# Kernel optimization log

Measured on AMD Instinct MI355X. Metric: run time of the kernel, lower is better.

The kernel has to match this reference:

```python
import jax, jax.numpy as jnp
import numpy as np

B, S, D_MODEL, D_K, D_V, H = 4, 2048, 1024, 1024, 1024, 16


def setup_inputs() -> dict:
    key = jax.random.key(0)
    ks = jax.random.split(key, 8)
    std_qk = np.sqrt(2.0 / (D_MODEL + D_K)).astype(np.float32)
    std_v = np.sqrt(2.0 / (D_MODEL + D_V)).astype(np.float32)
    std_o = np.sqrt(2.0 / (D_V + D_MODEL)).astype(np.float32)  # xavier normal
    return {
        "Q": jax.random.normal(ks[0], (B, S, D_MODEL), jnp.float32),
        "K": jax.random.normal(ks[1], (B, S, D_MODEL), jnp.float32),
        "V": jax.random.normal(ks[2], (B, S, D_MODEL), jnp.float32),
        "Wq": jax.random.normal(ks[3], (D_MODEL, D_K), jnp.float32) * std_qk,
        "bq": jnp.zeros((D_K,), jnp.float32),
        "Wk": jax.random.normal(ks[4], (D_MODEL, D_K), jnp.float32) * std_qk,
        "bk": jnp.zeros((D_K,), jnp.float32),
        "Wv": jax.random.normal(ks[5], (D_MODEL, D_V), jnp.float32) * std_v,
        "bv": jnp.zeros((D_V,), jnp.float32),
        "Wo": jax.random.normal(ks[6], (D_V, D_MODEL), jnp.float32) * std_o,
        "bo": jnp.zeros((D_MODEL,), jnp.float32),
    }


def reference(Q, K, V, Wq, bq, Wk, bk, Wv, bv, Wo, bo):
    b, s, _ = Q.shape
    hd = D_K // H  # per-head dim
    # separate QKV projections
    q = (Q @ Wq + bq).reshape(b, s, H, hd)
    k = (K @ Wk + bk).reshape(b, s, H, hd)
    v = (V @ Wv + bv).reshape(b, s, H, D_V // H)
    # scaled dot-product attention per head
    scale = 1.0 / jnp.sqrt(jnp.asarray(hd, Q.dtype))
    scores = jnp.einsum("bqhd,bkhd->bhqk", q, k) * scale
    attn = jax.nn.softmax(scores, axis=-1)
    o = jnp.einsum("bhqk,bkhd->bqhd", attn, v).reshape(b, s, D_V)
    # output projection
    return o @ Wo + bo
```

## Files before the change

kernel.cpp:

```cpp
#include <hip/hip_runtime.h>
#include <hip/hip_bf16.h>
#include <stdint.h>


#define B_  4
#define S_  2048
#define DM  1024
#define H_  16
#define HD  64
#define BH  (B_ * H_)

typedef __attribute__((ext_vector_type(8))) short short8;
typedef __attribute__((ext_vector_type(4))) float f32x4;

union U8 { short8 v; ushort u[8]; };

__device__ __forceinline__ ushort f2bf(float f) {
  union { float f; uint32_t i; } x; x.f = f;
  uint32_t r = (x.i + 0x7FFFu + ((x.i >> 16) & 1u)) >> 16;
  return (ushort)r;
}

__device__ __forceinline__ uint32_t cvt_pk_bf16(float a, float b) {
  uint32_t r;
  asm("v_cvt_pk_bf16_f32 %0, %1, %2" : "=v"(r) : "v"(a), "v"(b));
  return r;
}

__device__ __forceinline__ float exp2f_fast(float x) {
  float r;
  asm("v_exp_f32 %0, %1" : "=v"(r) : "v"(x));
  return r;
}

__device__ __forceinline__ void glds16(const ushort* g, ushort* l) {
  __builtin_amdgcn_global_load_lds(
      (const __attribute__((address_space(1))) void*)g,
      (__attribute__((address_space(3))) void*)l, 16, 0, 0);
}

#define MAX3(a, b, c) fmaxf(fmaxf((a), (b)), (c))

__global__ __launch_bounds__(256) void transposeW4(
    const float* __restrict__ s0, const float* __restrict__ s1,
    const float* __restrict__ s2, const float* __restrict__ s3,
    ushort* __restrict__ dbase) {
  __shared__ __align__(16) ushort tile[64][72];
  const int t = threadIdx.x;
  const int bx = blockIdx.x & 15;
  const int by = blockIdx.x >> 4;
  const int wsel = blockIdx.y;
  const float* src = wsel == 0 ? s0 : (wsel == 1 ? s1 : (wsel == 2 ? s2 : s3));
  ushort* dst = dbase + (size_t)wsel * 1024 * 1024;
#pragma unroll
  for (int i = 0; i < 2; i++) {
    int e = (i * 256 + t) * 8;
    int r = e >> 6, c = e & 63;
    const float* sp = src + (size_t)(by * 64 + r) * 1024 + bx * 64 + c;
    float4 a = ((const float4*)sp)[0];
    float4 b = ((const float4*)sp)[1];
    tile[r][c + 0] = f2bf(a.x); tile[r][c + 1] = f2bf(a.y);
    tile[r][c + 2] = f2bf(a.z); tile[r][c + 3] = f2bf(a.w);
    tile[r][c + 4] = f2bf(b.x); tile[r][c + 5] = f2bf(b.y);
    tile[r][c + 6] = f2bf(b.z); tile[r][c + 7] = f2bf(b.w);
  }
  __syncthreads();
#pragma unroll
  for (int i = 0; i < 2; i++) {
    int e = (i * 256 + t) * 8;
    int r = e >> 6, c = e & 63;
    U8 st;
#pragma unroll
    for (int j = 0; j < 8; j++) st.u[j] = tile[c + j][r];
    *(short8*)(dst + (size_t)(bx * 64 + r) * 1024 + by * 64 + c) = st.v;
  }
}


__global__ __launch_bounds__(256, 2) void gemm_qkv(
    const float* __restrict__ Qa, const float* __restrict__ Ka, const float* __restrict__ Va,
    const ushort* __restrict__ WT,
    const float* __restrict__ bq, const float* __restrict__ bk, const float* __restrict__ bv,
    ushort* __restrict__ qws, ushort* __restrict__ kws, ushort* __restrict__ vt) {
  __shared__ __align__(16) ushort lA[128 * 32];
  __shared__ __align__(16) ushort lB[128 * 32];
  const int z = blockIdx.z;
  const float* Ap = z == 0 ? Qa : (z == 1 ? Ka : Va);
  const ushort* BT = WT + (size_t)z * 1024 * 1024;
  const float* bias = z == 0 ? bq : (z == 1 ? bk : bv);
  const float oscale = z == 0 ? 0.18033688f : 1.0f;
  const int t = threadIdx.x;
  const int lane = t & 63;
  const int w = t >> 6;
  const int wr = w >> 1, wc = w & 1;
  const int bm0 = blockIdx.x * 128;
  const int bn0 = blockIdx.y * 128;
  f32x4 acc[4][4] = {};

  const int arow = t >> 2;
  const int acol = (t & 3) * 8;
  const int swz  = ((t & 3) ^ ((t >> 3) & 3)) * 8;
  const int rdo  = (((lane >> 4) ^ ((lane >> 1) & 3))) * 8;
  const float* fA0 = Ap + (size_t)(bm0 + arow) * 1024 + acol;
  const float* fA1 = Ap + (size_t)(bm0 + 64 + arow) * 1024 + acol;
  const ushort* gB0 = BT + (size_t)(bn0 + arow) * 1024 + swz;
  const ushort* gB1 = BT + (size_t)(bn0 + 64 + arow) * 1024 + swz;
  ushort* lAs0 = &lA[(t >> 2) * 32 + swz];
  ushort* lAs1 = &lA[2048 + (t >> 2) * 32 + swz];

  float4 px0 = ((const float4*)fA0)[0];
  float4 px1 = ((const float4*)fA0)[1];
  float4 py0 = ((const float4*)fA1)[0];
  float4 py1 = ((const float4*)fA1)[1];

  for (int k0 = 0; k0 < 1024; k0 += 32) {
    if (k0) __syncthreads();
    union { short8 v; uint32_t u[4]; } s0, s1;
    s0.u[0] = cvt_pk_bf16(px0.x, px0.y); s0.u[1] = cvt_pk_bf16(px0.z, px0.w);
    s0.u[2] = cvt_pk_bf16(px1.x, px1.y); s0.u[3] = cvt_pk_bf16(px1.z, px1.w);
    s1.u[0] = cvt_pk_bf16(py0.x, py0.y); s1.u[1] = cvt_pk_bf16(py0.z, py0.w);
    s1.u[2] = cvt_pk_bf16(py1.x, py1.y); s1.u[3] = cvt_pk_bf16(py1.z, py1.w);
    *(short8*)lAs0 = s0.v;
    *(short8*)lAs1 = s1.v;
    glds16(gB0 + k0, &lB[t * 8]);
    glds16(gB1 + k0, &lB[2048 + t * 8]);
    __syncthreads();
    if (k0 + 32 < 1024) {
      px0 = ((const float4*)(fA0 + k0 + 32))[0];
      px1 = ((const float4*)(fA0 + k0 + 32))[1];
      py0 = ((const float4*)(fA1 + k0 + 32))[0];
      py1 = ((const float4*)(fA1 + k0 + 32))[1];
    }
    short8 af[4], bf[4];
#pragma unroll
    for (int i = 0; i < 4; i++)
      af[i] = *(const short8*)&lA[(wr * 64 + i * 16 + (lane & 15)) * 32 + rdo];
#pragma unroll
    for (int j = 0; j < 4; j++)
      bf[j] = *(const short8*)&lB[(wc * 64 + j * 16 + (lane & 15)) * 32 + rdo];
#pragma unroll
    for (int i = 0; i < 4; i++)
#pragma unroll
      for (int j = 0; j < 4; j++)
        acc[i][j] = __builtin_amdgcn_mfma_f32_16x16x32_bf16(af[i], bf[j], acc[i][j], 0, 0, 0);
  }

  const int r0 = (lane >> 4) * 4;
#pragma unroll
  for (int j = 0; j < 4; j++) {
    const int col = bn0 + wc * 64 + j * 16 + (lane & 15);
    const float bc = bias[col];
#pragma unroll
    for (int i = 0; i < 4; i++) {
      const int row = bm0 + wr * 64 + i * 16 + r0;
      const int bb = row >> 11, s = row & 2047;
      const int hh = col >> 6, d = col & 63;
      if (z == 2) {
        uint32_t p01 = cvt_pk_bf16(acc[i][j][0] + bc, acc[i][j][1] + bc);
        uint32_t p23 = cvt_pk_bf16(acc[i][j][2] + bc, acc[i][j][3] + bc);
        ushort* vtb = vt + (((size_t)bb * H_ + hh) * HD + d) * (size_t)S_;
        const int sc = (s & 63) >> 2;
        *(uint2*)(vtb + (s & ~63) + ((sc ^ (d & 15)) << 2)) = (uint2){p01, p23};
      } else {
        ushort* dst = z == 0 ? qws : kws;
#pragma unroll
        for (int r = 0; r < 4; r++) {
          float val = (acc[i][j][r] + bc) * oscale;
          dst[(((size_t)bb * H_ + hh) * S_ + (s + r)) * HD + d] = f2bf(val);
        }
      }
    }
  }
}

__global__ __launch_bounds__(256, 2) void gemm_out(
    const ushort* __restrict__ Ap, const ushort* __restrict__ BT,
    const float* __restrict__ bias, float* __restrict__ Cp) {
  __shared__ __align__(16) ushort lA[128 * 32];
  __shared__ __align__(16) ushort lB[128 * 32];
  const int t = threadIdx.x;
  const int lane = t & 63;
  const int w = t >> 6;
  const int wr = w >> 1, wc = w & 1;
  const int bm0 = blockIdx.x * 128;
  const int bn0 = blockIdx.y * 128;
  f32x4 acc[4][4] = {};

  const int arow = t >> 2;
  const int swz  = ((t & 3) ^ ((t >> 3) & 3)) * 8;
  const int rdo  = (((lane >> 4) ^ ((lane >> 1) & 3))) * 8;
  const ushort* gA0 = Ap + (size_t)(bm0 + arow) * 1024 + swz;
  const ushort* gA1 = Ap + (size_t)(bm0 + 64 + arow) * 1024 + swz;
  const ushort* gB0 = BT + (size_t)(bn0 + arow) * 1024 + swz;
  const ushort* gB1 = BT + (size_t)(bn0 + 64 + arow) * 1024 + swz;

  for (int k0 = 0; k0 < 1024; k0 += 32) {
    if (k0) __syncthreads();
    glds16(gA0 + k0, &lA[t * 8]);
    glds16(gA1 + k0, &lA[2048 + t * 8]);
    glds16(gB0 + k0, &lB[t * 8]);
    glds16(gB1 + k0, &lB[2048 + t * 8]);
    __syncthreads();
    short8 af[4], bf[4];
#pragma unroll
    for (int i = 0; i < 4; i++)
      af[i] = *(const short8*)&lA[(wr * 64 + i * 16 + (lane & 15)) * 32 + rdo];
#pragma unroll
    for (int j = 0; j < 4; j++)
      bf[j] = *(const short8*)&lB[(wc * 64 + j * 16 + (lane & 15)) * 32 + rdo];
#pragma unroll
    for (int i = 0; i < 4; i++)
#pragma unroll
      for (int j = 0; j < 4; j++)
        acc[i][j] = __builtin_amdgcn_mfma_f32_16x16x32_bf16(af[i], bf[j], acc[i][j], 0, 0, 0);
  }

  const int r0 = (lane >> 4) * 4;
#pragma unroll
  for (int j = 0; j < 4; j++) {
    const int col = bn0 + wc * 64 + j * 16 + (lane & 15);
    const float bc = bias[col];
#pragma unroll
    for (int i = 0; i < 4; i++) {
      const int row = bm0 + wr * 64 + i * 16 + r0;
#pragma unroll
      for (int r = 0; r < 4; r++)
        Cp[(size_t)(row + r) * 1024 + col] = acc[i][j][r] + bc;
    }
  }
}

__global__ __launch_bounds__(256, 2) void attn(
    const ushort* __restrict__ q, const ushort* __restrict__ k,
    const ushort* __restrict__ vt, ushort* __restrict__ o) {
  __shared__ __align__(16) ushort kbuf[2][8192];
  __shared__ __align__(16) ushort vbuf[2][8192];
  const int t = threadIdx.x;
  const int lane = t & 63;
  const int w = t >> 6;
  const int L = ((blockIdx.x & 7) << 6) + (blockIdx.x >> 3);
  const int bh = L >> 3;
  const int q0 = (L & 7) * 256;
  const int b = bh >> 4, h = bh & 15;
  const int l15 = lane & 15;
  const int g = lane >> 4;

  const ushort* kbase  = k  + (size_t)bh * S_ * HD;
  const ushort* vtbase = vt + (size_t)bh * HD * S_;

  short8 qf[4][2];
#pragma unroll
  for (int qi = 0; qi < 4; qi++) {
    const ushort* qp = q + ((size_t)bh * S_ + q0 + w * 64 + qi * 16 + l15) * HD + g * 8;
    qf[qi][0] = *(const short8*)qp;
    qf[qi][1] = *(const short8*)(qp + 32);
  }

  short8 onesf;
#pragma unroll
  for (int j = 0; j < 8; j++) onesf[j] = (short)0x3F80;

  float m_r[4] = {-1e30f, -1e30f, -1e30f, -1e30f};
  f32x4 l_acc[4];
  f32x4 o_acc[4][4];
#pragma unroll
  for (int qi = 0; qi < 4; qi++) {
    l_acc[qi] = (f32x4){0.f, 0.f, 0.f, 0.f};
#pragma unroll
    for (int cb = 0; cb < 4; cb++) o_acc[qi][cb] = (f32x4){0.f, 0.f, 0.f, 0.f};
  }

  int vo[2][2];
#pragma unroll
  for (int ks = 0; ks < 2; ks++) {
    vo[ks][0] = ((8 * ks + g) ^ l15) << 2;
    vo[ks][1] = ((8 * ks + 4 + g) ^ l15) << 2;
  }

  auto STAGE = [&](int sel_, int kv0) {
#pragma unroll
    for (int i = 0; i < 4; i++) {
      int c = i * 256 + t;
      int krow = c >> 3;
      int kcc = (c & 7) ^ (krow & 7);
      glds16(kbase + (size_t)(kv0 + krow) * HD + kcc * 8, &kbuf[sel_][c * 8]);
      int d = c >> 4;
      int voff = ((c >> 3) & 1) * 64 + (c & 7) * 8;
      glds16(vtbase + (size_t)d * S_ + kv0 + voff, &vbuf[sel_][c * 8]);
    }
  };

  STAGE(0, 0);
  __syncthreads();

  int sel = 0;
  for (int kv0 = 0; kv0 < S_; kv0 += 128, sel ^= 1) {
    if (kv0 + 128 < S_) STAGE(sel ^ 1, kv0 + 128);

#pragma unroll
    for (int hb = 0; hb < 2; hb++) {
      f32x4 sc[4][4];
#pragma unroll
      for (int qi = 0; qi < 4; qi++)
#pragma unroll
        for (int cb = 0; cb < 4; cb++) sc[qi][cb] = (f32x4){0.f, 0.f, 0.f, 0.f};
#pragma unroll
      for (int cb = 0; cb < 4; cb++) {
        const int row = hb * 64 + cb * 16 + l15;
        const int r7 = row & 7;
        short8 kf0 = *(const short8*)&kbuf[sel][(row * 8 + (g ^ r7)) * 8];
        short8 kf1 = *(const short8*)&kbuf[sel][(row * 8 + ((4 + g) ^ r7)) * 8];
#pragma unroll
        for (int qi = 0; qi < 4; qi++) {
          sc[qi][cb] = __builtin_amdgcn_mfma_f32_16x16x32_bf16(kf0, qf[qi][0], sc[qi][cb], 0, 0, 0);
          sc[qi][cb] = __builtin_amdgcn_mfma_f32_16x16x32_bf16(kf1, qf[qi][1], sc[qi][cb], 0, 0, 0);
        }
      }

      union PB { short8 v; uint32_t u[4]; } pbq[4][2];
#pragma unroll
      for (int qi = 0; qi < 4; qi++) {
        const float m = m_r[qi];
#pragma unroll
        for (int cb = 0; cb < 4; cb++) {
          float p0 = exp2f_fast(sc[qi][cb][0] - m);
          float p1 = exp2f_fast(sc[qi][cb][1] - m);
          float p2 = exp2f_fast(sc[qi][cb][2] - m);
          float p3 = exp2f_fast(sc[qi][cb][3] - m);
          pbq[qi][cb >> 1].u[(cb & 1) * 2 + 0] = cvt_pk_bf16(p0, p1);
          pbq[qi][cb >> 1].u[(cb & 1) * 2 + 1] = cvt_pk_bf16(p2, p3);
        }
        float z0 = MAX3(sc[qi][0][0], sc[qi][0][1], sc[qi][0][2]);
        float z1 = MAX3(sc[qi][0][3], sc[qi][1][0], sc[qi][1][1]);
        float z2 = MAX3(sc[qi][1][2], sc[qi][1][3], sc[qi][2][0]);
        float z3 = MAX3(sc[qi][2][1], sc[qi][2][2], sc[qi][2][3]);
        float z4 = MAX3(sc[qi][3][0], sc[qi][3][1], sc[qi][3][2]);
        float mx = MAX3(MAX3(z0, z1, z2), fmaxf(z3, z4), sc[qi][3][3]);
        mx = fmaxf(mx, __shfl_xor(mx, 16));
        mx = fmaxf(mx, __shfl_xor(mx, 32));

        const float THR = 11.5415603f;
        if (!__all(mx <= m + THR)) {
          float mn = fmaxf(m, mx);
          float fct = exp2f_fast(m - mn);
          m_r[qi] = mn;
          l_acc[qi] *= fct;
#pragma unroll
          for (int cb = 0; cb < 4; cb++)
#pragma unroll
            for (int r = 0; r < 4; r++) o_acc[qi][cb][r] *= fct;
#pragma unroll
          for (int cb = 0; cb < 4; cb++) {
            float p0 = exp2f_fast(sc[qi][cb][0] - mn);
            float p1 = exp2f_fast(sc[qi][cb][1] - mn);
            float p2 = exp2f_fast(sc[qi][cb][2] - mn);
            float p3 = exp2f_fast(sc[qi][cb][3] - mn);
            pbq[qi][cb >> 1].u[(cb & 1) * 2 + 0] = cvt_pk_bf16(p0, p1);
            pbq[qi][cb >> 1].u[(cb & 1) * 2 + 1] = cvt_pk_bf16(p2, p3);
          }
        }
      }

#pragma unroll
      for (int ks = 0; ks < 2; ks++) {
#pragma unroll
        for (int qi = 0; qi < 4; qi++)
          l_acc[qi] = __builtin_amdgcn_mfma_f32_16x16x32_bf16(onesf, pbq[qi][ks].v, l_acc[qi], 0, 0, 0);
#pragma unroll
        for (int cb = 0; cb < 4; cb++) {
          const ushort* vb = &vbuf[sel][(cb * 16 + l15) * 128 + hb * 64];
          union { short8 v; uint2 d2[2]; } vv;
          vv.d2[0] = *(const uint2*)(vb + vo[ks][0]);
          vv.d2[1] = *(const uint2*)(vb + vo[ks][1]);
#pragma unroll
          for (int qi = 0; qi < 4; qi++)
            o_acc[qi][cb] = __builtin_amdgcn_mfma_f32_16x16x32_bf16(vv.v, pbq[qi][ks].v, o_acc[qi][cb], 0, 0, 0);
        }
      }
    }
    __syncthreads();
  }

#pragma unroll
  for (int qi = 0; qi < 4; qi++) {
    const float inv = 1.f / l_acc[qi][0];
    ushort* ob = o + ((size_t)b * S_ + q0 + w * 64 + qi * 16 + l15) * DM + h * HD + 4 * g;
#pragma unroll
    for (int cb = 0; cb < 4; cb++) {
      uint2 st;
      st.x = cvt_pk_bf16(o_acc[qi][cb][0] * inv, o_acc[qi][cb][1] * inv);
      st.y = cvt_pk_bf16(o_acc[qi][cb][2] * inv, o_acc[qi][cb][3] * inv);
      *(uint2*)(ob + cb * 16) = st;
    }
  }
}

extern "C" void kernel_launch(void* const* d_in, const int* in_sizes, int n_in,
                              void* d_out, int out_size, void* d_ws, size_t ws_size,
                              hipStream_t stream) {
  const float* Q  = (const float*)d_in[0];
  const float* K  = (const float*)d_in[1];
  const float* V  = (const float*)d_in[2];
  const float* Wq = (const float*)d_in[3];
  const float* bq = (const float*)d_in[4];
  const float* Wk = (const float*)d_in[5];
  const float* bk = (const float*)d_in[6];
  const float* Wv = (const float*)d_in[7];
  const float* bv = (const float*)d_in[8];
  const float* Wo = (const float*)d_in[9];
  const float* bo = (const float*)d_in[10];
  float* out = (float*)d_out;
  ushort* ws = (ushort*)d_ws;

  const size_t WN = (size_t)1024 * 1024;
  const size_t PN = (size_t)B_ * S_ * DM;
  ushort* wT  = ws;
  ushort* woT = ws + 3 * WN;
  ushort* qws = ws + 4 * WN;
  ushort* kws = qws + PN;
  ushort* ows = kws + PN;
  ushort* vt  = (ushort*)d_out;

  transposeW4<<<dim3(256, 4), 256, 0, stream>>>(Wq, Wk, Wv, Wo, wT);

  gemm_qkv<<<dim3(64, 8, 3), 256, 0, stream>>>(Q, K, V, wT, bq, bk, bv, qws, kws, vt);

  attn<<<BH * 8, 256, 0, stream>>>(qws, kws, vt, ows);

  gemm_out<<<dim3(64, 8), 256, 0, stream>>>(ows, woT, bo, out);
}
```

Before: 190.3 us.

## Split attention KV range across two wave groups and merge partial softmax

```diff
diff --git a/kernel.cpp b/kernel.cpp
--- a/kernel.cpp
+++ b/kernel.cpp
@@ -230,14 +230,15 @@
   }
 }
 
-__global__ __launch_bounds__(256, 2) void attn(
+__global__ __launch_bounds__(512, 4) void attn(
     const ushort* __restrict__ q, const ushort* __restrict__ k,
     const ushort* __restrict__ vt, ushort* __restrict__ o) {
-  __shared__ __align__(16) ushort kbuf[2][8192];
-  __shared__ __align__(16) ushort vbuf[2][8192];
+  __shared__ __align__(16) ushort smem[32768];
   const int t = threadIdx.x;
   const int lane = t & 63;
   const int w = t >> 6;
+  const int wq = w & 3;
+  const int kvh = w >> 2;
   const int L = ((blockIdx.x & 7) << 6) + (blockIdx.x >> 3);
   const int bh = L >> 3;
   const int q0 = (L & 7) * 256;
@@ -251,7 +252,7 @@
   short8 qf[4][2];
 #pragma unroll
   for (int qi = 0; qi < 4; qi++) {
-    const ushort* qp = q + ((size_t)bh * S_ + q0 + w * 64 + qi * 16 + l15) * HD + g * 8;
+    const ushort* qp = q + ((size_t)bh * S_ + q0 + wq * 64 + qi * 16 + l15) * HD + g * 8;
     qf[qi][0] = *(const short8*)qp;
     qf[qi][1] = *(const short8*)(qp + 32);
   }
@@ -278,119 +279,162 @@
   }
 
   auto STAGE = [&](int sel_, int kv0) {
-#pragma unroll
-    for (int i = 0; i < 4; i++) {
-      int c = i * 256 + t;
-      int krow = c >> 3;
-      int kcc = (c & 7) ^ (krow & 7);
-      glds16(kbase + (size_t)(kv0 + krow) * HD + kcc * 8, &kbuf[sel_][c * 8]);
-      int d = c >> 4;
-      int voff = ((c >> 3) & 1) * 64 + (c & 7) * 8;
-      glds16(vtbase + (size_t)d * S_ + kv0 + voff, &vbuf[sel_][c * 8]);
+    const int tt = t & 255;
+#pragma unroll
+    for (int i = 0; i < 2; i++) {
+      int c = i * 256 + tt;
+      int row = c >> 3;
+      int cc = (c & 7) ^ (row & 7);
+      glds16(kbase + (size_t)(kv0 + row) * HD + cc * 8, &smem[kvh * 8192 + sel_ * 4096 + c * 8]);
+      glds16(vtbase + (size_t)row * S_ + kv0 + (c & 7) * 8,
+             &smem[16384 + kvh * 8192 + sel_ * 4096 + c * 8]);
     }
   };
 
-  STAGE(0, 0);
+  const int kvstart = kvh * 1024;
+  STAGE(0, kvstart);
   __syncthreads();
 
   int sel = 0;
-  for (int kv0 = 0; kv0 < S_; kv0 += 128, sel ^= 1) {
-    if (kv0 + 128 < S_) STAGE(sel ^ 1, kv0 + 128);
-
-#pragma unroll
-    for (int hb = 0; hb < 2; hb++) {
-      f32x4 sc[4][4];
-#pragma unroll
-      for (int qi = 0; qi < 4; qi++)
-#pragma unroll
-        for (int cb = 0; cb < 4; cb++) sc[qi][cb] = (f32x4){0.f, 0.f, 0.f, 0.f};
+  for (int r = 0; r < 16; r++, sel ^= 1) {
+    const int kv0 = kvstart + r * 64;
+    if (r + 1 < 16) STAGE(sel ^ 1, kv0 + 64);
+    const ushort* kb  = &smem[kvh * 8192 + sel * 4096];
+    const ushort* vbb = &smem[16384 + kvh * 8192 + sel * 4096];
+
+    f32x4 sc[4][4];
+#pragma unroll
+    for (int qi = 0; qi < 4; qi++)
+#pragma unroll
+      for (int cb = 0; cb < 4; cb++) sc[qi][cb] = (f32x4){0.f, 0.f, 0.f, 0.f};
+#pragma unroll
+    for (int cb = 0; cb < 4; cb++) {
+      const int row = cb * 16 + l15;
+      const int r7 = row & 7;
+      short8 kf0 = *(const short8*)&kb[(row * 8 + (g ^ r7)) * 8];
+      short8 kf1 = *(const short8*)&kb[(row * 8 + ((4 + g) ^ r7)) * 8];
+#pragma unroll
+      for (int qi = 0; qi < 4; qi++) {
+        sc[qi][cb] = __builtin_amdgcn_mfma_f32_16x16x32_bf16(kf0, qf[qi][0], sc[qi][cb], 0, 0, 0);
+        sc[qi][cb] = __builtin_amdgcn_mfma_f32_16x16x32_bf16(kf1, qf[qi][1], sc[qi][cb], 0, 0, 0);
+      }
+    }
+
+    union PB { short8 v; uint32_t u[4]; } pbq[4][2];
+#pragma unroll
+    for (int qi = 0; qi < 4; qi++) {
+      const float m = m_r[qi];
 #pragma unroll
       for (int cb = 0; cb < 4; cb++) {
-        const int row = hb * 64 + cb * 16 + l15;
-        const int r7 = row & 7;
-        short8 kf0 = *(const short8*)&kbuf[sel][(row * 8 + (g ^ r7)) * 8];
-        short8 kf1 = *(const short8*)&kbuf[sel][(row * 8 + ((4 + g) ^ r7)) * 8];
-#pragma unroll
-        for (int qi = 0; qi < 4; qi++) {
-          sc[qi][cb] = __builtin_amdgcn_mfma_f32_16x16x32_bf16(kf0, qf[qi][0], sc[qi][cb], 0, 0, 0);
-          sc[qi][cb] = __builtin_amdgcn_mfma_f32_16x16x32_bf16(kf1, qf[qi][1], sc[qi][cb], 0, 0, 0);
-        }
-      }
-
-      union PB { short8 v; uint32_t u[4]; } pbq[4][2];
-#pragma unroll
-      for (int qi = 0; qi < 4; qi++) {
-        const float m = m_r[qi];
+        float p0 = exp2f_fast(sc[qi][cb][0] - m);
+        float p1 = exp2f_fast(sc[qi][cb][1] - m);
+        float p2 = exp2f_fast(sc[qi][cb][2] - m);
+        float p3 = exp2f_fast(sc[qi][cb][3] - m);
+        pbq[qi][cb >> 1].u[(cb & 1) * 2 + 0] = cvt_pk_bf16(p0, p1);
+        pbq[qi][cb >> 1].u[(cb & 1) * 2 + 1] = cvt_pk_bf16(p2, p3);
+      }
+      float z0 = MAX3(sc[qi][0][0], sc[qi][0][1], sc[qi][0][2]);
+      float z1 = MAX3(sc[qi][0][3], sc[qi][1][0], sc[qi][1][1]);
+      float z2 = MAX3(sc[qi][1][2], sc[qi][1][3], sc[qi][2][0]);
+      float z3 = MAX3(sc[qi][2][1], sc[qi][2][2], sc[qi][2][3]);
+      float z4 = MAX3(sc[qi][3][0], sc[qi][3][1], sc[qi][3][2]);
+      float mx = MAX3(MAX3(z0, z1, z2), fmaxf(z3, z4), sc[qi][3][3]);
+      mx = fmaxf(mx, __shfl_xor(mx, 16));
+      mx = fmaxf(mx, __shfl_xor(mx, 32));
+
+      const float THR = 11.5415603f;
+      if (!__all(mx <= m + THR)) {
+        float mn = fmaxf(m, mx);
+        float fct = exp2f_fast(m - mn);
+        m_r[qi] = mn;
+        l_acc[qi] *= fct;
+#pragma unroll
+        for (int cb = 0; cb < 4; cb++)
+#pragma unroll
+          for (int rr = 0; rr < 4; rr++) o_acc[qi][cb][rr] *= fct;
 #pragma unroll
         for (int cb = 0; cb < 4; cb++) {
-          float p0 = exp2f_fast(sc[qi][cb][0] - m);
-          float p1 = exp2f_fast(sc[qi][cb][1] - m);
-          float p2 = exp2f_fast(sc[qi][cb][2] - m);
-          float p3 = exp2f_fast(sc[qi][cb][3] - m);
+          float p0 = exp2f_fast(sc[qi][cb][0] - mn);
+          float p1 = exp2f_fast(sc[qi][cb][1] - mn);
+          float p2 = exp2f_fast(sc[qi][cb][2] - mn);
+          float p3 = exp2f_fast(sc[qi][cb][3] - mn);
           pbq[qi][cb >> 1].u[(cb & 1) * 2 + 0] = cvt_pk_bf16(p0, p1);
           pbq[qi][cb >> 1].u[(cb & 1) * 2 + 1] = cvt_pk_bf16(p2, p3);
         }
-        float z0 = MAX3(sc[qi][0][0], sc[qi][0][1], sc[qi][0][2]);
-        float z1 = MAX3(sc[qi][0][3], sc[qi][1][0], sc[qi][1][1]);
-        float z2 = MAX3(sc[qi][1][2], sc[qi][1][3], sc[qi][2][0]);
-        float z3 = MAX3(sc[qi][2][1], sc[qi][2][2], sc[qi][2][3]);
-        float z4 = MAX3(sc[qi][3][0], sc[qi][3][1], sc[qi][3][2]);
-        float mx = MAX3(MAX3(z0, z1, z2), fmaxf(z3, z4), sc[qi][3][3]);
-        mx = fmaxf(mx, __shfl_xor(mx, 16));
-        mx = fmaxf(mx, __shfl_xor(mx, 32));
-
-        const float THR = 11.5415603f;
-        if (!__all(mx <= m + THR)) {
-          float mn = fmaxf(m, mx);
-          float fct = exp2f_fast(m - mn);
-          m_r[qi] = mn;
-          l_acc[qi] *= fct;
-#pragma unroll
-          for (int cb = 0; cb < 4; cb++)
-#pragma unroll
-            for (int r = 0; r < 4; r++) o_acc[qi][cb][r] *= fct;
-#pragma unroll
-          for (int cb = 0; cb < 4; cb++) {
-            float p0 = exp2f_fast(sc[qi][cb][0] - mn);
-            float p1 = exp2f_fast(sc[qi][cb][1] - mn);
-            float p2 = exp2f_fast(sc[qi][cb][2] - mn);
-            float p3 = exp2f_fast(sc[qi][cb][3] - mn);
-            pbq[qi][cb >> 1].u[(cb & 1) * 2 + 0] = cvt_pk_bf16(p0, p1);
-            pbq[qi][cb >> 1].u[(cb & 1) * 2 + 1] = cvt_pk_bf16(p2, p3);
-          }
-        }
-      }
-
-#pragma unroll
-      for (int ks = 0; ks < 2; ks++) {
+      }
+    }
+
+#pragma unroll
+    for (int ks = 0; ks < 2; ks++) {
+#pragma unroll
+      for (int qi = 0; qi < 4; qi++)
+        l_acc[qi] = __builtin_amdgcn_mfma_f32_16x16x32_bf16(onesf, pbq[qi][ks].v, l_acc[qi], 0, 0, 0);
+#pragma unroll
+      for (int cb = 0; cb < 4; cb++) {
+        const ushort* vb = &vbb[(cb * 16 + l15) * 64];
+        union { short8 v; uint2 d2[2]; } vv;
+        vv.d2[0] = *(const uint2*)(vb + vo[ks][0]);
+        vv.d2[1] = *(const uint2*)(vb + vo[ks][1]);
 #pragma unroll
         for (int qi = 0; qi < 4; qi++)
-          l_acc[qi] = __builtin_amdgcn_mfma_f32_16x16x32_bf16(onesf, pbq[qi][ks].v, l_acc[qi], 0, 0, 0);
-#pragma unroll
-        for (int cb = 0; cb < 4; cb++) {
-          const ushort* vb = &vbuf[sel][(cb * 16 + l15) * 128 + hb * 64];
-          union { short8 v; uint2 d2[2]; } vv;
-          vv.d2[0] = *(const uint2*)(vb + vo[ks][0]);
-          vv.d2[1] = *(const uint2*)(vb + vo[ks][1]);
-#pragma unroll
-          for (int qi = 0; qi < 4; qi++)
-            o_acc[qi][cb] = __builtin_amdgcn_mfma_f32_16x16x32_bf16(vv.v, pbq[qi][ks].v, o_acc[qi][cb], 0, 0, 0);
-        }
+          o_acc[qi][cb] = __builtin_amdgcn_mfma_f32_16x16x32_bf16(vv.v, pbq[qi][ks].v, o_acc[qi][cb], 0, 0, 0);
       }
     }
     __syncthreads();
   }
 
-#pragma unroll
-  for (int qi = 0; qi < 4; qi++) {
-    const float inv = 1.f / l_acc[qi][0];
-    ushort* ob = o + ((size_t)b * S_ + q0 + w * 64 + qi * 16 + l15) * DM + h * HD + 4 * g;
-#pragma unroll
-    for (int cb = 0; cb < 4; cb++) {
-      uint2 st;
-      st.x = cvt_pk_bf16(o_acc[qi][cb][0] * inv, o_acc[qi][cb][1] * inv);
-      st.y = cvt_pk_bf16(o_acc[qi][cb][2] * inv, o_acc[qi][cb][3] * inv);
-      *(uint2*)(ob + cb * 16) = st;
+  float* xf = (float*)smem;
+#pragma unroll
+  for (int p = 0; p < 2; p++) {
+    if (w >= 4) {
+      const int slot = ((w - 4) * 64 + lane) * 37;
+#pragma unroll
+      for (int qq = 0; qq < 2; qq++) {
+        const int qi = p * 2 + qq;
+#pragma unroll
+        for (int cb = 0; cb < 4; cb++)
+#pragma unroll
+          for (int rr = 0; rr < 4; rr++)
+            xf[slot + qq * 16 + cb * 4 + rr] = o_acc[qi][cb][rr];
+        xf[slot + 32 + qq] = l_acc[qi][0];
+        xf[slot + 34 + qq] = m_r[qi];
+      }
+    }
+    __syncthreads();
+    if (w < 4) {
+      const int slot = (w * 64 + lane) * 37;
+#pragma unroll
+      for (int qq = 0; qq < 2; qq++) {
+        const int qi = p * 2 + qq;
+        const float mb = xf[slot + 34 + qq];
+        const float lb = xf[slot + 32 + qq];
+        const float mn = fmaxf(m_r[qi], mb);
+        const float fa = exp2f_fast(m_r[qi] - mn);
+        const float fb = exp2f_fast(mb - mn);
+        m_r[qi] = mn;
+        l_acc[qi][0] = l_acc[qi][0] * fa + lb * fb;
+#pragma unroll
+        for (int cb = 0; cb < 4; cb++)
+#pragma unroll
+          for (int rr = 0; rr < 4; rr++)
+            o_acc[qi][cb][rr] = o_acc[qi][cb][rr] * fa + xf[slot + qq * 16 + cb * 4 + rr] * fb;
+      }
+    }
+    __syncthreads();
+  }
+
+  if (w < 4) {
+#pragma unroll
+    for (int qi = 0; qi < 4; qi++) {
+      const float inv = 1.f / l_acc[qi][0];
+      ushort* ob = o + ((size_t)b * S_ + q0 + wq * 64 + qi * 16 + l15) * DM + h * HD + 4 * g;
+#pragma unroll
+      for (int cb = 0; cb < 4; cb++) {
+        uint2 st;
+        st.x = cvt_pk_bf16(o_acc[qi][cb][0] * inv, o_acc[qi][cb][1] * inv);
+        st.y = cvt_pk_bf16(o_acc[qi][cb][2] * inv, o_acc[qi][cb][3] * inv);
+        *(uint2*)(ob + cb * 16) = st;
+      }
     }
   }
 }
@@ -425,7 +469,7 @@
 
   gemm_qkv<<<dim3(64, 8, 3), 256, 0, stream>>>(Q, K, V, wT, bq, bk, bv, qws, kws, vt);
 
-  attn<<<BH * 8, 256, 0, stream>>>(qws, kws, vt, ows);
+  attn<<<BH * 8, 512, 0, stream>>>(qws, kws, vt, ows);
 
   gemm_out<<<dim3(64, 8), 256, 0, stream>>>(ows, woT, bo, out);
 }
```

Result: slower. 594.3 us (+212.2%).

## Load K and V tiles directly from global memory in attention, dropping LDS staging

Applied to the files above, without the earlier changes.

```diff
diff --git a/kernel.cpp b/kernel.cpp
--- a/kernel.cpp
+++ b/kernel.cpp
@@ -159,8 +159,7 @@
         uint32_t p01 = cvt_pk_bf16(acc[i][j][0] + bc, acc[i][j][1] + bc);
         uint32_t p23 = cvt_pk_bf16(acc[i][j][2] + bc, acc[i][j][3] + bc);
         ushort* vtb = vt + (((size_t)bb * H_ + hh) * HD + d) * (size_t)S_;
-        const int sc = (s & 63) >> 2;
-        *(uint2*)(vtb + (s & ~63) + ((sc ^ (d & 15)) << 2)) = (uint2){p01, p23};
+        *(uint2*)(vtb + s) = (uint2){p01, p23};
       } else {
         ushort* dst = z == 0 ? qws : kws;
 #pragma unroll
@@ -233,8 +232,6 @@
 __global__ __launch_bounds__(256, 2) void attn(
     const ushort* __restrict__ q, const ushort* __restrict__ k,
     const ushort* __restrict__ vt, ushort* __restrict__ o) {
-  __shared__ __align__(16) ushort kbuf[2][8192];
-  __shared__ __align__(16) ushort vbuf[2][8192];
   const int t = threadIdx.x;
   const int lane = t & 63;
   const int w = t >> 6;
@@ -270,115 +267,87 @@
     for (int cb = 0; cb < 4; cb++) o_acc[qi][cb] = (f32x4){0.f, 0.f, 0.f, 0.f};
   }
 
-  int vo[2][2];
-#pragma unroll
-  for (int ks = 0; ks < 2; ks++) {
-    vo[ks][0] = ((8 * ks + g) ^ l15) << 2;
-    vo[ks][1] = ((8 * ks + 4 + g) ^ l15) << 2;
-  }
-
-  auto STAGE = [&](int sel_, int kv0) {
-#pragma unroll
-    for (int i = 0; i < 4; i++) {
-      int c = i * 256 + t;
-      int krow = c >> 3;
-      int kcc = (c & 7) ^ (krow & 7);
-      glds16(kbase + (size_t)(kv0 + krow) * HD + kcc * 8, &kbuf[sel_][c * 8]);
-      int d = c >> 4;
-      int voff = ((c >> 3) & 1) * 64 + (c & 7) * 8;
-      glds16(vtbase + (size_t)d * S_ + kv0 + voff, &vbuf[sel_][c * 8]);
-    }
-  };
-
-  STAGE(0, 0);
-  __syncthreads();
-
-  int sel = 0;
-  for (int kv0 = 0; kv0 < S_; kv0 += 128, sel ^= 1) {
-    if (kv0 + 128 < S_) STAGE(sel ^ 1, kv0 + 128);
-
-#pragma unroll
-    for (int hb = 0; hb < 2; hb++) {
-      f32x4 sc[4][4];
-#pragma unroll
-      for (int qi = 0; qi < 4; qi++)
-#pragma unroll
-        for (int cb = 0; cb < 4; cb++) sc[qi][cb] = (f32x4){0.f, 0.f, 0.f, 0.f};
+  const ushort* krow0 = kbase + (size_t)l15 * HD + g * 8;
+  const ushort* vrow0 = vtbase + (size_t)l15 * S_;
+
+  for (int kv0 = 0; kv0 < S_; kv0 += 64) {
+    f32x4 sc[4][4];
+#pragma unroll
+    for (int qi = 0; qi < 4; qi++)
+#pragma unroll
+      for (int cb = 0; cb < 4; cb++) sc[qi][cb] = (f32x4){0.f, 0.f, 0.f, 0.f};
+#pragma unroll
+    for (int cb = 0; cb < 4; cb++) {
+      const ushort* kp = krow0 + (size_t)(kv0 + cb * 16) * HD;
+      short8 kf0 = *(const short8*)kp;
+      short8 kf1 = *(const short8*)(kp + 32);
+#pragma unroll
+      for (int qi = 0; qi < 4; qi++) {
+        sc[qi][cb] = __builtin_amdgcn_mfma_f32_16x16x32_bf16(kf0, qf[qi][0], sc[qi][cb], 0, 0, 0);
+        sc[qi][cb] = __builtin_amdgcn_mfma_f32_16x16x32_bf16(kf1, qf[qi][1], sc[qi][cb], 0, 0, 0);
+      }
+    }
+
+    union PB { short8 v; uint32_t u[4]; } pbq[4][2];
+#pragma unroll
+    for (int qi = 0; qi < 4; qi++) {
+      const float m = m_r[qi];
 #pragma unroll
       for (int cb = 0; cb < 4; cb++) {
-        const int row = hb * 64 + cb * 16 + l15;
-        const int r7 = row & 7;
-        short8 kf0 = *(const short8*)&kbuf[sel][(row * 8 + (g ^ r7)) * 8];
-        short8 kf1 = *(const short8*)&kbuf[sel][(row * 8 + ((4 + g) ^ r7)) * 8];
-#pragma unroll
-        for (int qi = 0; qi < 4; qi++) {
-          sc[qi][cb] = __builtin_amdgcn_mfma_f32_16x16x32_bf16(kf0, qf[qi][0], sc[qi][cb], 0, 0, 0);
-          sc[qi][cb] = __builtin_amdgcn_mfma_f32_16x16x32_bf16(kf1, qf[qi][1], sc[qi][cb], 0, 0, 0);
-        }
+        float p0 = exp2f_fast(sc[qi][cb][0] - m);
+        float p1 = exp2f_fast(sc[qi][cb][1] - m);
+        float p2 = exp2f_fast(sc[qi][cb][2] - m);
+        float p3 = exp2f_fast(sc[qi][cb][3] - m);
+        pbq[qi][cb >> 1].u[(cb & 1) * 2 + 0] = cvt_pk_bf16(p0, p1);
+        pbq[qi][cb >> 1].u[(cb & 1) * 2 + 1] = cvt_pk_bf16(p2, p3);
       }
-
-      union PB { short8 v; uint32_t u[4]; } pbq[4][2];
-#pragma unroll
-      for (int qi = 0; qi < 4; qi++) {
-        const float m = m_r[qi];
+      float z0 = MAX3(sc[qi][0][0], sc[qi][0][1], sc[qi][0][2]);
+      float z1 = MAX3(sc[qi][0][3], sc[qi][1][0], sc[qi][1][1]);
+      float z2 = MAX3(sc[qi][1][2], sc[qi][1][3], sc[qi][2][0]);
+      float z3 = MAX3(sc[qi][2][1], sc[qi][2][2], sc[qi][2][3]);
+      float z4 = MAX3(sc[qi][3][0], sc[qi][3][1], sc[qi][3][2]);
+      float mx = MAX3(MAX3(z0, z1, z2), fmaxf(z3, z4), sc[qi][3][3]);
+      mx = fmaxf(mx, __shfl_xor(mx, 16));
+      mx = fmaxf(mx, __shfl_xor(mx, 32));
+
+      const float THR = 11.5415603f;
+      if (!__all(mx <= m + THR)) {
+        float mn = fmaxf(m, mx);
+        float fct = exp2f_fast(m - mn);
+        m_r[qi] = mn;
+        l_acc[qi] *= fct;
+#pragma unroll
+        for (int cb = 0; cb < 4; cb++)
+#pragma unroll
+          for (int rr = 0; rr < 4; rr++) o_acc[qi][cb][rr] *= fct;
 #pragma unroll
         for (int cb = 0; cb < 4; cb++) {
-          float p0 = exp2f_fast(sc[qi][cb][0] - m);
-          float p1 = exp2f_fast(sc[qi][cb][1] - m);
-          float p2 = exp2f_fast(sc[qi][cb][2] - m);
-          float p3 = exp2f_fast(sc[qi][cb][3] - m);
+          float p0 = exp2f_fast(sc[qi][cb][0] - mn);
+          float p1 = exp2f_fast(sc[qi][cb][1] - mn);
+          float p2 = exp2f_fast(sc[qi][cb][2] - mn);
+          float p3 = exp2f_fast(sc[qi][cb][3] - mn);
           pbq[qi][cb >> 1].u[(cb & 1) * 2 + 0] = cvt_pk_bf16(p0, p1);
           pbq[qi][cb >> 1].u[(cb & 1) * 2 + 1] = cvt_pk_bf16(p2, p3);
         }
-        float z0 = MAX3(sc[qi][0][0], sc[qi][0][1], sc[qi][0][2]);
-        float z1 = MAX3(sc[qi][0][3], sc[qi][1][0], sc[qi][1][1]);
-        float z2 = MAX3(sc[qi][1][2], sc[qi][1][3], sc[qi][2][0]);
-        float z3 = MAX3(sc[qi][2][1], sc[qi][2][2], sc[qi][2][3]);
-        float z4 = MAX3(sc[qi][3][0], sc[qi][3][1], sc[qi][3][2]);
-        float mx = MAX3(MAX3(z0, z1, z2), fmaxf(z3, z4), sc[qi][3][3]);
-        mx = fmaxf(mx, __shfl_xor(mx, 16));
-        mx = fmaxf(mx, __shfl_xor(mx, 32));
-
-        const float THR = 11.5415603f;
-        if (!__all(mx <= m + THR)) {
-          float mn = fmaxf(m, mx);
-          float fct = exp2f_fast(m - mn);
-          m_r[qi] = mn;
-          l_acc[qi] *= fct;
-#pragma unroll
-          for (int cb = 0; cb < 4; cb++)
-#pragma unroll
-            for (int r = 0; r < 4; r++) o_acc[qi][cb][r] *= fct;
-#pragma unroll
-          for (int cb = 0; cb < 4; cb++) {
-            float p0 = exp2f_fast(sc[qi][cb][0] - mn);
-            float p1 = exp2f_fast(sc[qi][cb][1] - mn);
-            float p2 = exp2f_fast(sc[qi][cb][2] - mn);
-            float p3 = exp2f_fast(sc[qi][cb][3] - mn);
-            pbq[qi][cb >> 1].u[(cb & 1) * 2 + 0] = cvt_pk_bf16(p0, p1);
-            pbq[qi][cb >> 1].u[(cb & 1) * 2 + 1] = cvt_pk_bf16(p2, p3);
-          }
-        }
       }
-
-#pragma unroll
-      for (int ks = 0; ks < 2; ks++) {
+    }
+
+#pragma unroll
+    for (int ks = 0; ks < 2; ks++) {
+#pragma unroll
+      for (int qi = 0; qi < 4; qi++)
+        l_acc[qi] = __builtin_amdgcn_mfma_f32_16x16x32_bf16(onesf, pbq[qi][ks].v, l_acc[qi], 0, 0, 0);
+#pragma unroll
+      for (int cb = 0; cb < 4; cb++) {
+        const ushort* vp = vrow0 + (size_t)(cb * 16) * S_ + kv0;
+        union { short8 v; uint2 d2[2]; } vv;
+        vv.d2[0] = *(const uint2*)(vp + (8 * ks + g) * 4);
+        vv.d2[1] = *(const uint2*)(vp + (8 * ks + 4 + g) * 4);
 #pragma unroll
         for (int qi = 0; qi < 4; qi++)
-          l_acc[qi] = __builtin_amdgcn_mfma_f32_16x16x32_bf16(onesf, pbq[qi][ks].v, l_acc[qi], 0, 0, 0);
-#pragma unroll
-        for (int cb = 0; cb < 4; cb++) {
-          const ushort* vb = &vbuf[sel][(cb * 16 + l15) * 128 + hb * 64];
-          union { short8 v; uint2 d2[2]; } vv;
-          vv.d2[0] = *(const uint2*)(vb + vo[ks][0]);
-          vv.d2[1] = *(const uint2*)(vb + vo[ks][1]);
-#pragma unroll
-          for (int qi = 0; qi < 4; qi++)
-            o_acc[qi][cb] = __builtin_amdgcn_mfma_f32_16x16x32_bf16(vv.v, pbq[qi][ks].v, o_acc[qi][cb], 0, 0, 0);
-        }
+          o_acc[qi][cb] = __builtin_amdgcn_mfma_f32_16x16x32_bf16(vv.v, pbq[qi][ks].v, o_acc[qi][cb], 0, 0, 0);
       }
     }
-    __syncthreads();
   }
 
 #pragma unroll
```

Result: slower. 290.0 us (+52.3%).

## Stage K/V through registers with 64-wide KV tiles instead of direct LDS loads

Applied to the files above, without the earlier changes.

```diff
diff --git a/kernel.cpp b/kernel.cpp
--- a/kernel.cpp
+++ b/kernel.cpp
@@ -233,8 +233,8 @@
 __global__ __launch_bounds__(256, 2) void attn(
     const ushort* __restrict__ q, const ushort* __restrict__ k,
     const ushort* __restrict__ vt, ushort* __restrict__ o) {
-  __shared__ __align__(16) ushort kbuf[2][8192];
-  __shared__ __align__(16) ushort vbuf[2][8192];
+  __shared__ __align__(16) ushort kbuf[2][4096];
+  __shared__ __align__(16) ushort vbuf[2][4096];
   const int t = threadIdx.x;
   const int lane = t & 63;
   const int w = t >> 6;
@@ -277,107 +277,118 @@
     vo[ks][1] = ((8 * ks + 4 + g) ^ l15) << 2;
   }
 
-  auto STAGE = [&](int sel_, int kv0) {
-#pragma unroll
-    for (int i = 0; i < 4; i++) {
-      int c = i * 256 + t;
-      int krow = c >> 3;
-      int kcc = (c & 7) ^ (krow & 7);
-      glds16(kbase + (size_t)(kv0 + krow) * HD + kcc * 8, &kbuf[sel_][c * 8]);
-      int d = c >> 4;
-      int voff = ((c >> 3) & 1) * 64 + (c & 7) * 8;
-      glds16(vtbase + (size_t)d * S_ + kv0 + voff, &vbuf[sel_][c * 8]);
-    }
+  const int c0 = t, c1 = 256 + t;
+  const int kr0 = c0 >> 3, kc0 = c0 & 7;
+  const int kr1 = c1 >> 3, kc1 = c1 & 7;
+  const int kp0 = (c0 & ~7) | (kc0 ^ (kr0 & 7));
+  const int kp1 = (c1 & ~7) | (kc1 ^ (kr1 & 7));
+  const ushort* gk0 = kbase + (size_t)kr0 * HD + kc0 * 8;
+  const ushort* gk1 = kbase + (size_t)kr1 * HD + kc1 * 8;
+  const ushort* gv0 = vtbase + (size_t)kr0 * S_ + kc0 * 8;
+  const ushort* gv1 = vtbase + (size_t)kr1 * S_ + kc1 * 8;
+  uint4 rk0, rk1, rv0, rv1;
+  auto LOADR = [&](int kv0) {
+    rk0 = *(const uint4*)(gk0 + (size_t)kv0 * HD);
+    rk1 = *(const uint4*)(gk1 + (size_t)kv0 * HD);
+    rv0 = *(const uint4*)(gv0 + kv0);
+    rv1 = *(const uint4*)(gv1 + kv0);
   };
-
-  STAGE(0, 0);
+  auto WRITE = [&](int sel_) {
+    *(uint4*)&kbuf[sel_][kp0 * 8] = rk0;
+    *(uint4*)&kbuf[sel_][kp1 * 8] = rk1;
+    *(uint4*)&vbuf[sel_][c0 * 8] = rv0;
+    *(uint4*)&vbuf[sel_][c1 * 8] = rv1;
+  };
+
+  LOADR(0);
+  WRITE(0);
   __syncthreads();
 
   int sel = 0;
-  for (int kv0 = 0; kv0 < S_; kv0 += 128, sel ^= 1) {
-    if (kv0 + 128 < S_) STAGE(sel ^ 1, kv0 + 128);
-
-#pragma unroll
-    for (int hb = 0; hb < 2; hb++) {
-      f32x4 sc[4][4];
-#pragma unroll
-      for (int qi = 0; qi < 4; qi++)
-#pragma unroll
-        for (int cb = 0; cb < 4; cb++) sc[qi][cb] = (f32x4){0.f, 0.f, 0.f, 0.f};
+  for (int kv0 = 0; kv0 < S_; kv0 += 64, sel ^= 1) {
+    const int more = (kv0 + 64 < S_);
+    if (more) LOADR(kv0 + 64);
+
+    f32x4 sc[4][4];
+#pragma unroll
+    for (int qi = 0; qi < 4; qi++)
+#pragma unroll
+      for (int cb = 0; cb < 4; cb++) sc[qi][cb] = (f32x4){0.f, 0.f, 0.f, 0.f};
+#pragma unroll
+    for (int cb = 0; cb < 4; cb++) {
+      const int row = cb * 16 + l15;
+      const int r7 = row & 7;
+      short8 kf0 = *(const short8*)&kbuf[sel][(row * 8 + (g ^ r7)) * 8];
+      short8 kf1 = *(const short8*)&kbuf[sel][(row * 8 + ((4 + g) ^ r7)) * 8];
+#pragma unroll
+      for (int qi = 0; qi < 4; qi++) {
+        sc[qi][cb] = __builtin_amdgcn_mfma_f32_16x16x32_bf16(kf0, qf[qi][0], sc[qi][cb], 0, 0, 0);
+        sc[qi][cb] = __builtin_amdgcn_mfma_f32_16x16x32_bf16(kf1, qf[qi][1], sc[qi][cb], 0, 0, 0);
+      }
+    }
+
+    union PB { short8 v; uint32_t u[4]; } pbq[4][2];
+#pragma unroll
+    for (int qi = 0; qi < 4; qi++) {
+      const float m = m_r[qi];
 #pragma unroll
       for (int cb = 0; cb < 4; cb++) {
-        const int row = hb * 64 + cb * 16 + l15;
-        const int r7 = row & 7;
-        short8 kf0 = *(const short8*)&kbuf[sel][(row * 8 + (g ^ r7)) * 8];
-        short8 kf1 = *(const short8*)&kbuf[sel][(row * 8 + ((4 + g) ^ r7)) * 8];
-#pragma unroll
-        for (int qi = 0; qi < 4; qi++) {
-          sc[qi][cb] = __builtin_amdgcn_mfma_f32_16x16x32_bf16(kf0, qf[qi][0], sc[qi][cb], 0, 0, 0);
-          sc[qi][cb] = __builtin_amdgcn_mfma_f32_16x16x32_bf16(kf1, qf[qi][1], sc[qi][cb], 0, 0, 0);
-        }
+        float p0 = exp2f_fast(sc[qi][cb][0] - m);
+        float p1 = exp2f_fast(sc[qi][cb][1] - m);
+        float p2 = exp2f_fast(sc[qi][cb][2] - m);
+        float p3 = exp2f_fast(sc[qi][cb][3] - m);
+        pbq[qi][cb >> 1].u[(cb & 1) * 2 + 0] = cvt_pk_bf16(p0, p1);
+        pbq[qi][cb >> 1].u[(cb & 1) * 2 + 1] = cvt_pk_bf16(p2, p3);
       }
-
-      union PB { short8 v; uint32_t u[4]; } pbq[4][2];
-#pragma unroll
-      for (int qi = 0; qi < 4; qi++) {
-        const float m = m_r[qi];
+      float z0 = MAX3(sc[qi][0][0], sc[qi][0][1], sc[qi][0][2]);
+      float z1 = MAX3(sc[qi][0][3], sc[qi][1][0], sc[qi][1][1]);
+      float z2 = MAX3(sc[qi][1][2], sc[qi][1][3], sc[qi][2][0]);
+      float z3 = MAX3(sc[qi][2][1], sc[qi][2][2], sc[qi][2][3]);
+      float z4 = MAX3(sc[qi][3][0], sc[qi][3][1], sc[qi][3][2]);
+      float mx = MAX3(MAX3(z0, z1, z2), fmaxf(z3, z4), sc[qi][3][3]);
+      mx = fmaxf(mx, __shfl_xor(mx, 16));
+      mx = fmaxf(mx, __shfl_xor(mx, 32));
+
+      const float THR = 11.5415603f;
+      if (!__all(mx <= m + THR)) {
+        float mn = fmaxf(m, mx);
+        float fct = exp2f_fast(m - mn);
+        m_r[qi] = mn;
+        l_acc[qi] *= fct;
+#pragma unroll
+        for (int cb = 0; cb < 4; cb++)
+#pragma unroll
+          for (int rr = 0; rr < 4; rr++) o_acc[qi][cb][rr] *= fct;
 #pragma unroll
         for (int cb = 0; cb < 4; cb++) {
-          float p0 = exp2f_fast(sc[qi][cb][0] - m);
-          float p1 = exp2f_fast(sc[qi][cb][1] - m);
-          float p2 = exp2f_fast(sc[qi][cb][2] - m);
-          float p3 = exp2f_fast(sc[qi][cb][3] - m);
+          float p0 = exp2f_fast(sc[qi][cb][0] - mn);
+          float p1 = exp2f_fast(sc[qi][cb][1] - mn);
+          float p2 = exp2f_fast(sc[qi][cb][2] - mn);
+          float p3 = exp2f_fast(sc[qi][cb][3] - mn);
           pbq[qi][cb >> 1].u[(cb & 1) * 2 + 0] = cvt_pk_bf16(p0, p1);
           pbq[qi][cb >> 1].u[(cb & 1) * 2 + 1] = cvt_pk_bf16(p2, p3);
         }
-        float z0 = MAX3(sc[qi][0][0], sc[qi][0][1], sc[qi][0][2]);
-        float z1 = MAX3(sc[qi][0][3], sc[qi][1][0], sc[qi][1][1]);
-        float z2 = MAX3(sc[qi][1][2], sc[qi][1][3], sc[qi][2][0]);
-        float z3 = MAX3(sc[qi][2][1], sc[qi][2][2], sc[qi][2][3]);
-        float z4 = MAX3(sc[qi][3][0], sc[qi][3][1], sc[qi][3][2]);
-        float mx = MAX3(MAX3(z0, z1, z2), fmaxf(z3, z4), sc[qi][3][3]);
-        mx = fmaxf(mx, __shfl_xor(mx, 16));
-        mx = fmaxf(mx, __shfl_xor(mx, 32));
-
-        const float THR = 11.5415603f;
-        if (!__all(mx <= m + THR)) {
-          float mn = fmaxf(m, mx);
-          float fct = exp2f_fast(m - mn);
-          m_r[qi] = mn;
-          l_acc[qi] *= fct;
-#pragma unroll
-          for (int cb = 0; cb < 4; cb++)
-#pragma unroll
-            for (int r = 0; r < 4; r++) o_acc[qi][cb][r] *= fct;
-#pragma unroll
-          for (int cb = 0; cb < 4; cb++) {
-            float p0 = exp2f_fast(sc[qi][cb][0] - mn);
-            float p1 = exp2f_fast(sc[qi][cb][1] - mn);
-            float p2 = exp2f_fast(sc[qi][cb][2] - mn);
-            float p3 = exp2f_fast(sc[qi][cb][3] - mn);
-            pbq[qi][cb >> 1].u[(cb & 1) * 2 + 0] = cvt_pk_bf16(p0, p1);
-            pbq[qi][cb >> 1].u[(cb & 1) * 2 + 1] = cvt_pk_bf16(p2, p3);
-          }
-        }
       }
-
-#pragma unroll
-      for (int ks = 0; ks < 2; ks++) {
+    }
+
+#pragma unroll
+    for (int ks = 0; ks < 2; ks++) {
+#pragma unroll
+      for (int qi = 0; qi < 4; qi++)
+        l_acc[qi] = __builtin_amdgcn_mfma_f32_16x16x32_bf16(onesf, pbq[qi][ks].v, l_acc[qi], 0, 0, 0);
+#pragma unroll
+      for (int cb = 0; cb < 4; cb++) {
+        const ushort* vb = &vbuf[sel][(cb * 16 + l15) * 64];
+        union { short8 v; uint2 d2[2]; } vv;
+        vv.d2[0] = *(const uint2*)(vb + vo[ks][0]);
+        vv.d2[1] = *(const uint2*)(vb + vo[ks][1]);
 #pragma unroll
         for (int qi = 0; qi < 4; qi++)
-          l_acc[qi] = __builtin_amdgcn_mfma_f32_16x16x32_bf16(onesf, pbq[qi][ks].v, l_acc[qi], 0, 0, 0);
-#pragma unroll
-        for (int cb = 0; cb < 4; cb++) {
-          const ushort* vb = &vbuf[sel][(cb * 16 + l15) * 128 + hb * 64];
-          union { short8 v; uint2 d2[2]; } vv;
-          vv.d2[0] = *(const uint2*)(vb + vo[ks][0]);
-          vv.d2[1] = *(const uint2*)(vb + vo[ks][1]);
-#pragma unroll
-          for (int qi = 0; qi < 4; qi++)
-            o_acc[qi][cb] = __builtin_amdgcn_mfma_f32_16x16x32_bf16(vv.v, pbq[qi][ks].v, o_acc[qi][cb], 0, 0, 0);
-        }
+          o_acc[qi][cb] = __builtin_amdgcn_mfma_f32_16x16x32_bf16(vv.v, pbq[qi][ks].v, o_acc[qi][cb], 0, 0, 0);
       }
     }
+
+    if (more) WRITE(sel ^ 1);
     __syncthreads();
   }
 
```

After: 192.3 us. No clear change (+1.1%).
